# Kernel optimization log

Measured on AMD Instinct MI355X. Metric: run time of the kernel, lower is better.

The kernel has to match this reference:

```python
import jax, jax.numpy as jnp
import numpy as np

# Fixed intrinsics from PhotometricLoss.__init__
W, H = 640, 480
FU, FV = 320.0, 320.0
CU, CV = (W - 1) / 2.0, (H - 1) / 2.0  # cu,cv default to (dim-1)/2
BASELINE = 0.25  # t_vec = [0.25, 0, 0], r_mat = I


def _grid_sample_bilinear_zeros(img, grid):
    """torch.F.grid_sample(img, grid) with bilinear interp, zeros padding,
    align_corners=False (modern torch default).
    img: [B,C,H,W], grid: [B,H,W,2] (x,y) in [-1,1]. Returns [B,C,H,W]."""
    B, C, Hh, Ww = img.shape
    gx, gy = grid[..., 0], grid[..., 1]
    # unnormalize (align_corners=False)
    x = ((gx + 1.0) * Ww - 1.0) * 0.5
    y = ((gy + 1.0) * Hh - 1.0) * 0.5
    x0 = jnp.floor(x)
    y0 = jnp.floor(y)
    wx1 = x - x0
    wy1 = y - y0
    wx0 = 1.0 - wx1
    wy0 = 1.0 - wy1
    b = jnp.arange(B)[:, None, None]

    def gather(yi, xi):
        valid = (xi >= 0) & (xi < Ww) & (yi >= 0) & (yi < Hh)
        xi_c = jnp.clip(xi, 0, Ww - 1).astype(jnp.int32)
        yi_c = jnp.clip(yi, 0, Hh - 1).astype(jnp.int32)
        v = img[b, :, yi_c, xi_c]  # [B,H,W,C]
        return v * valid[..., None].astype(img.dtype)

    out = (gather(y0, x0) * (wy0 * wx0)[..., None]
           + gather(y0, x0 + 1) * (wy0 * wx1)[..., None]
           + gather(y0 + 1, x0) * (wy1 * wx0)[..., None]
           + gather(y0 + 1, x0 + 1) * (wy1 * wx1)[..., None])
    return jnp.transpose(out, (0, 3, 1, 2))  # [B,C,H,W]


def setup_inputs() -> dict:
    key = jax.random.key(0)
    k1, k2, k3 = jax.random.split(key, 3)
    Bsz = 32
    rgb_right = jax.random.uniform(k1, (Bsz, 3, H, W), jnp.float32) * 255.0
    rgb_left = jax.random.uniform(k2, (Bsz, 3, H, W), jnp.float32) * 255.0
    # depth in [1, 80] meters -> disparity fu*B/Z in [1, 80] pixels
    depth_right = jax.random.uniform(k3, (Bsz, 1, H, W), jnp.float32) * 79.0 + 1.0
    return {"rgb_right": rgb_right, "rgb_left": rgb_left, "depth_right": depth_right}


def reference(rgb_right, rgb_left, depth_right):
    # camera rays (X_cam, Y_cam) from Intrinsics
    u = jnp.arange(W, dtype=jnp.float32)
    v = jnp.arange(H, dtype=jnp.float32)
    X_cam = (u[None, :] - CU) / FU  # [1,W] -> broadcasts over H
    Y_cam = (v[:, None] - CV) / FV  # [H,1]

    d = depth_right[:, 0]  # [B,H,W]
    # image_to_pointcloud + transform_curr_to_near (R = I, t = [BASELINE,0,0])
    X = d * X_cam + BASELINE
    Y = d * Y_cam
    Z = jnp.maximum(d, 0.001)  # clamp(min=0.001)

    # pointcloud_to_image
    U_proj = FU * X / Z + CU
    V_proj = FV * Y / Z + CV
    un = 2.0 * U_proj / (W - 1) - 1.0
    vn = 2.0 * V_proj / (H - 1) - 1.0
    un = jnp.where(jnp.abs(un) > 1.0, 2.0, un)  # out-of-frame -> 2 (zeros padding)
    vn = jnp.where(jnp.abs(vn) > 1.0, 2.0, vn)
    grid = jnp.stack([un, vn], axis=-1)  # [B,H,W,2]

    warped = _grid_sample_bilinear_zeros(rgb_left, grid)  # [B,3,H,W]

    diff = jnp.sum(jnp.abs(warped - rgb_right), axis=1)  # [B,H,W]
    valid_mask = ((jnp.sum(warped, axis=1) > 0)
                  & (jnp.sum(rgb_left, axis=1) > 0)).astype(diff.dtype)
    return jnp.mean(diff * valid_mask)
```

## Files before the change

### kernel.cpp

```cpp
#include <hip/hip_runtime.h>

#define IMG_W 640
#define IMG_H 480
#define BATCH 32
#define HWSZ (IMG_H * IMG_W)
#define CHWSZ (3 * HWSZ)
#define NPIX (BATCH * HWSZ)

#define GROUPS_PER_ROW (IMG_W / 4)
#define NROWS (BATCH * IMG_H)
#define NGROUPS (NROWS * GROUPS_PER_ROW)
#define NTHREADS 256
#define NBLOCKS (NGROUPS / NTHREADS)

__global__ __launch_bounds__(NTHREADS) void photo_main(
    const float* __restrict__ rgb_right,
    const float* __restrict__ rgb_left,
    const float* __restrict__ depth,
    float* __restrict__ partials)
{
    const int g = blockIdx.x * NTHREADS + threadIdx.x;
    const int row = g / GROUPS_PER_ROW;
    const int u4 = (g - row * GROUPS_PER_ROW) * 4;
    const int b = row / IMG_H;
    const int v = row - b * IMG_H;

    const size_t dbase = (size_t)b * HWSZ + (size_t)v * IMG_W + u4;
    const size_t rbase = (size_t)b * CHWSZ + (size_t)v * IMG_W + u4;

    const float4 d4 = *(const float4*)(depth + dbase);
    const float4 r0 = *(const float4*)(rgb_right + rbase);
    const float4 r1 = *(const float4*)(rgb_right + rbase + HWSZ);
    const float4 r2 = *(const float4*)(rgb_right + rbase + 2 * HWSZ);

    const float darr[4] = {d4.x, d4.y, d4.z, d4.w};
    const float R0[4] = {r0.x, r0.y, r0.z, r0.w};
    const float R1[4] = {r1.x, r1.y, r1.z, r1.w};
    const float R2[4] = {r2.x, r2.y, r2.z, r2.w};

    const float* __restrict__ Lb = rgb_left + (size_t)b * CHWSZ;

    const float Yc = ((float)v - 239.5f) * (1.0f / 320.0f);

    float acc = 0.0f;

#pragma unroll
    for (int j = 0; j < 4; ++j) {
        const float dd = darr[j];
        const float uf = (float)(u4 + j);

        const float Xc = (uf - 319.5f) * (1.0f / 320.0f);
        const float X = dd * Xc + 0.25f;
        const float Y = dd * Yc;
        const float Z = fmaxf(dd, 0.001f);
        const float rz = __builtin_amdgcn_rcpf(Z);
        const float Up = 320.0f * X * rz + 319.5f;
        const float Vp = 320.0f * Y * rz + 239.5f;

        float un = 2.0f * Up * (1.0f / 639.0f) - 1.0f;
        float vn = 2.0f * Vp * (1.0f / 479.0f) - 1.0f;
        un = (fabsf(un) > 1.0f) ? 2.0f : un;
        vn = (fabsf(vn) > 1.0f) ? 2.0f : vn;

        const float x = ((un + 1.0f) * (float)IMG_W - 1.0f) * 0.5f;
        const float y = ((vn + 1.0f) * (float)IMG_H - 1.0f) * 0.5f;
        const float x0f = floorf(x);
        const float y0f = floorf(y);
        const float wx1 = x - x0f;
        const float wy1 = y - y0f;
        const float wx0 = 1.0f - wx1;
        const float wy0 = 1.0f - wy1;
        const int x0 = (int)x0f, y0 = (int)y0f;
        const int x1 = x0 + 1,   y1 = y0 + 1;

        const bool vx0 = (x0 >= 0) & (x0 < IMG_W);
        const bool vx1 = (x1 >= 0) & (x1 < IMG_W);
        const bool vy0 = (y0 >= 0) & (y0 < IMG_H);
        const bool vy1 = (y1 >= 0) & (y1 < IMG_H);
        const int cx0 = min(max(x0, 0), IMG_W - 1);
        const int cx1 = min(max(x1, 0), IMG_W - 1);
        const int cy0 = min(max(y0, 0), IMG_H - 1);
        const int cy1 = min(max(y1, 0), IMG_H - 1);

        const float w00 = wy0 * wx0 * ((vy0 & vx0) ? 1.0f : 0.0f);
        const float w01 = wy0 * wx1 * ((vy0 & vx1) ? 1.0f : 0.0f);
        const float w10 = wy1 * wx0 * ((vy1 & vx0) ? 1.0f : 0.0f);
        const float w11 = wy1 * wx1 * ((vy1 & vx1) ? 1.0f : 0.0f);

        const int i00 = cy0 * IMG_W + cx0;
        const int i01 = cy0 * IMG_W + cx1;
        const int i10 = cy1 * IMG_W + cx0;
        const int i11 = cy1 * IMG_W + cx1;

        const float* p00 = Lb + i00;
        const float* p01 = Lb + i01;
        const float* p10 = Lb + i10;
        const float* p11 = Lb + i11;

        const float a00 = p00[0],        a01 = p01[0],        a10 = p10[0],        a11 = p11[0];
        const float b00 = p00[HWSZ],     b01 = p01[HWSZ],     b10 = p10[HWSZ],     b11 = p11[HWSZ];
        const float c00 = p00[2 * HWSZ], c01 = p01[2 * HWSZ], c10 = p10[2 * HWSZ], c11 = p11[2 * HWSZ];

        const float wa = w00 * a00 + w01 * a01 + w10 * a10 + w11 * a11;
        const float wb = w00 * b00 + w01 * b01 + w10 * b10 + w11 * b11;
        const float wc = w00 * c00 + w01 * c01 + w10 * c10 + w11 * c11;

        const float wsum = wa + wb + wc;
        const float diff = fabsf(wa - R0[j]) + fabsf(wb - R1[j]) + fabsf(wc - R2[j]);

        acc += (wsum > 0.0f) ? diff : 0.0f;
    }

    for (int off = 32; off > 0; off >>= 1)
        acc += __shfl_down(acc, off, 64);

    __shared__ float lds[NTHREADS / 64];
    const int lane = threadIdx.x & 63;
    const int wave = threadIdx.x >> 6;
    if (lane == 0) lds[wave] = acc;
    __syncthreads();
    if (threadIdx.x == 0) {
        float s = 0.0f;
#pragma unroll
        for (int w = 0; w < NTHREADS / 64; ++w) s += lds[w];
        partials[blockIdx.x] = s;
    }
}

__global__ __launch_bounds__(1024) void photo_finish(
    const float* __restrict__ partials,
    float* __restrict__ out,
    int nb)
{
    double s = 0.0;
    for (int i = threadIdx.x; i < nb; i += blockDim.x)
        s += (double)partials[i];

    for (int off = 32; off > 0; off >>= 1)
        s += __shfl_down(s, off, 64);

    __shared__ double lds[16];
    const int lane = threadIdx.x & 63;
    const int wave = threadIdx.x >> 6;
    if (lane == 0) lds[wave] = s;
    __syncthreads();
    if (threadIdx.x == 0) {
        double t = 0.0;
#pragma unroll
        for (int w = 0; w < 16; ++w) t += lds[w];
        out[0] = (float)(t / (double)NPIX);
    }
}

extern "C" void kernel_launch(void* const* d_in, const int* in_sizes, int n_in,
                              void* d_out, int out_size, void* d_ws, size_t ws_size,
                              hipStream_t stream) {
    const float* rgb_right = (const float*)d_in[0];
    const float* rgb_left  = (const float*)d_in[1];
    const float* depth     = (const float*)d_in[2];
    float* partials = (float*)d_ws;
    float* out = (float*)d_out;

    photo_main<<<NBLOCKS, NTHREADS, 0, stream>>>(rgb_right, rgb_left, depth, partials);
    photo_finish<<<1, 1024, 0, stream>>>(partials, out, NBLOCKS);
}
```

Before: 296.8 us.

## Stage the two needed left-image rows in LDS per output row

With identity rotation and a pure x baseline, the projected vertical coordinate equals the pixel row whenever depth exceeds the clamp. The kernel therefore now launches one block per output row and cooperatively loads the two source rows (all three channels) of the left image into shared memory. Bilinear taps then read from LDS instead of doing scattered global gathers, and per-pixel loads become scalar coalesced loads. The shortcut relies on depth being at least 0.001 (true for valid depth), and it clamps the row offsets for pixels whose computed row differs slightly from the staged rows.

```diff
diff --git a/kernel.cpp b/kernel.cpp
--- a/kernel.cpp
+++ b/kernel.cpp
@@ -7,11 +7,8 @@
 #define CHWSZ (3 * HWSZ)
 #define NPIX (BATCH * HWSZ)
 
-#define GROUPS_PER_ROW (IMG_W / 4)
 #define NROWS (BATCH * IMG_H)
-#define NGROUPS (NROWS * GROUPS_PER_ROW)
-#define NTHREADS 256
-#define NBLOCKS (NGROUPS / NTHREADS)
+#define NTHREADS 320
 
 __global__ __launch_bounds__(NTHREADS) void photo_main(
     const float* __restrict__ rgb_right,
@@ -19,37 +16,48 @@
     const float* __restrict__ depth,
     float* __restrict__ partials)
 {
-    const int g = blockIdx.x * NTHREADS + threadIdx.x;
-    const int row = g / GROUPS_PER_ROW;
-    const int u4 = (g - row * GROUPS_PER_ROW) * 4;
-    const int b = row / IMG_H;
-    const int v = row - b * IMG_H;
+    const int rowid = blockIdx.x;
+    const int b = rowid / IMG_H;
+    const int v = rowid - b * IMG_H;
 
-    const size_t dbase = (size_t)b * HWSZ + (size_t)v * IMG_W + u4;
-    const size_t rbase = (size_t)b * CHWSZ + (size_t)v * IMG_W + u4;
+    const float yrow = (480.0f * (float)v) / 479.0f - 0.5f;
+    const int y0s = (int)floorf(yrow);
+    const int r0 = min(max(y0s, 0), IMG_H - 1);
+    const int r1 = min(max(y0s + 1, 0), IMG_H - 1);
 
-    const float4 d4 = *(const float4*)(depth + dbase);
-    const float4 r0 = *(const float4*)(rgb_right + rbase);
-    const float4 r1 = *(const float4*)(rgb_right + rbase + HWSZ);
-    const float4 r2 = *(const float4*)(rgb_right + rbase + 2 * HWSZ);
-
-    const float darr[4] = {d4.x, d4.y, d4.z, d4.w};
-    const float R0[4] = {r0.x, r0.y, r0.z, r0.w};
-    const float R1[4] = {r1.x, r1.y, r1.z, r1.w};
-    const float R2[4] = {r2.x, r2.y, r2.z, r2.w};
+    __shared__ float lds[2 * 3 * IMG_W];
 
     const float* __restrict__ Lb = rgb_left + (size_t)b * CHWSZ;
 
+#pragma unroll
+    for (int k = 0; k < 3; ++k) {
+        const int idx = threadIdx.x + k * NTHREADS;
+        const int rowch = idx / 160;
+        const int x4 = idx - rowch * 160;
+        const int rowsel = (rowch >= 3) ? 1 : 0;
+        const int c = rowch - 3 * rowsel;
+        const int rsrc = rowsel ? r1 : r0;
+        const float4 val = *(const float4*)(Lb + (size_t)c * HWSZ + (size_t)rsrc * IMG_W + 4 * x4);
+        *(float4*)(&lds[rowch * IMG_W + 4 * x4]) = val;
+    }
+    __syncthreads();
+
+    const size_t dbase = (size_t)b * HWSZ + (size_t)v * IMG_W;
+    const size_t rbase = (size_t)b * CHWSZ + (size_t)v * IMG_W;
     const float Yc = ((float)v - 239.5f) * (1.0f / 320.0f);
 
     float acc = 0.0f;
 
 #pragma unroll
-    for (int j = 0; j < 4; ++j) {
-        const float dd = darr[j];
-        const float uf = (float)(u4 + j);
+    for (int i = 0; i < 2; ++i) {
+        const int u = threadIdx.x + i * NTHREADS;
 
-        const float Xc = (uf - 319.5f) * (1.0f / 320.0f);
+        const float dd = depth[dbase + u];
+        const float Rr = rgb_right[rbase + u];
+        const float Rg = rgb_right[rbase + HWSZ + u];
+        const float Rb2 = rgb_right[rbase + 2 * HWSZ + u];
+
+        const float Xc = ((float)u - 319.5f) * (1.0f / 320.0f);
         const float X = dd * Xc + 0.25f;
         const float Y = dd * Yc;
         const float Z = fmaxf(dd, 0.001f);
@@ -79,34 +87,29 @@
         const bool vy1 = (y1 >= 0) & (y1 < IMG_H);
         const int cx0 = min(max(x0, 0), IMG_W - 1);
         const int cx1 = min(max(x1, 0), IMG_W - 1);
-        const int cy0 = min(max(y0, 0), IMG_H - 1);
-        const int cy1 = min(max(y1, 0), IMG_H - 1);
 
         const float w00 = wy0 * wx0 * ((vy0 & vx0) ? 1.0f : 0.0f);
         const float w01 = wy0 * wx1 * ((vy0 & vx1) ? 1.0f : 0.0f);
         const float w10 = wy1 * wx0 * ((vy1 & vx0) ? 1.0f : 0.0f);
         const float w11 = wy1 * wx1 * ((vy1 & vx1) ? 1.0f : 0.0f);
 
-        const int i00 = cy0 * IMG_W + cx0;
-        const int i01 = cy0 * IMG_W + cx1;
-        const int i10 = cy1 * IMG_W + cx0;
-        const int i11 = cy1 * IMG_W + cx1;
+        const int s0 = min(max(y0 - y0s, 0), 1) * (3 * IMG_W);
+        const int s1 = min(max(y1 - y0s, 0), 1) * (3 * IMG_W);
 
-        const float* p00 = Lb + i00;
-        const float* p01 = Lb + i01;
-        const float* p10 = Lb + i10;
-        const float* p11 = Lb + i11;
-
-        const float a00 = p00[0],        a01 = p01[0],        a10 = p10[0],        a11 = p11[0];
-        const float b00 = p00[HWSZ],     b01 = p01[HWSZ],     b10 = p10[HWSZ],     b11 = p11[HWSZ];
-        const float c00 = p00[2 * HWSZ], c01 = p01[2 * HWSZ], c10 = p10[2 * HWSZ], c11 = p11[2 * HWSZ];
-
-        const float wa = w00 * a00 + w01 * a01 + w10 * a10 + w11 * a11;
-        const float wb = w00 * b00 + w01 * b01 + w10 * b10 + w11 * b11;
-        const float wc = w00 * c00 + w01 * c01 + w10 * c10 + w11 * c11;
-
-        const float wsum = wa + wb + wc;
-        const float diff = fabsf(wa - R0[j]) + fabsf(wb - R1[j]) + fabsf(wc - R2[j]);
+        float wsum = 0.0f;
+        float diff = 0.0f;
+#pragma unroll
+        for (int c = 0; c < 3; ++c) {
+            const int cb = c * IMG_W;
+            const float t00 = lds[s0 + cb + cx0];
+            const float t01 = lds[s0 + cb + cx1];
+            const float t10 = lds[s1 + cb + cx0];
+            const float t11 = lds[s1 + cb + cx1];
+            const float w = w00 * t00 + w01 * t01 + w10 * t10 + w11 * t11;
+            const float r = (c == 0) ? Rr : ((c == 1) ? Rg : Rb2);
+            wsum += w;
+            diff += fabsf(w - r);
+        }
 
         acc += (wsum > 0.0f) ? diff : 0.0f;
     }
@@ -114,15 +117,15 @@
     for (int off = 32; off > 0; off >>= 1)
         acc += __shfl_down(acc, off, 64);
 
-    __shared__ float lds[NTHREADS / 64];
+    __shared__ float red[NTHREADS / 64];
     const int lane = threadIdx.x & 63;
     const int wave = threadIdx.x >> 6;
-    if (lane == 0) lds[wave] = acc;
+    if (lane == 0) red[wave] = acc;
     __syncthreads();
     if (threadIdx.x == 0) {
         float s = 0.0f;
 #pragma unroll
-        for (int w = 0; w < NTHREADS / 64; ++w) s += lds[w];
+        for (int w = 0; w < NTHREADS / 64; ++w) s += red[w];
         partials[blockIdx.x] = s;
     }
 }
@@ -161,6 +164,6 @@
     float* partials = (float*)d_ws;
     float* out = (float*)d_out;
 
-    photo_main<<<NBLOCKS, NTHREADS, 0, stream>>>(rgb_right, rgb_left, depth, partials);
-    photo_finish<<<1, 1024, 0, stream>>>(partials, out, NBLOCKS);
+    photo_main<<<NROWS, NTHREADS, 0, stream>>>(rgb_right, rgb_left, depth, partials);
+    photo_finish<<<1, 1024, 0, stream>>>(partials, out, NROWS);
 }
```

New measurement: 280.3 us. -5.6%, faster.
